# Kernel tuning notes

Measured on AMD Instinct MI355X. Metric: run time of the kernel, lower is better.

Reference implementation:

```python
import jax, jax.numpy as jnp
import numpy as np
import math

NUM_HEADS = 16
D_EMBED = 1024
D_HEAD = D_EMBED // NUM_HEADS


def setup_inputs() -> dict:
    key = jax.random.key(0)
    k1, k2, k3 = jax.random.split(key, 3)
    B, S = 4, 2048
    x = jax.random.normal(k1, (B, S, D_EMBED), dtype=jnp.float32)
    # Kaiming-ish init for the fused QKV and output projections
    scale_in = 1.0 / math.sqrt(D_EMBED)
    in_proj_weight = jax.random.normal(k2, (3 * D_EMBED, D_EMBED), dtype=jnp.float32) * scale_in
    out_proj_weight = jax.random.normal(k3, (D_EMBED, D_EMBED), dtype=jnp.float32) * scale_in
    return {
        "x": x,
        "in_proj_weight": in_proj_weight,
        "out_proj_weight": out_proj_weight,
        "causal_mask": 1,
    }


def reference(x, in_proj_weight, out_proj_weight, causal_mask):
    B, S, D = x.shape
    # fused QKV projection: x @ W_in^T -> [B, S, 3D], then split
    qkv = jnp.einsum("bsd,ed->bse", x, in_proj_weight)
    q, k, v = jnp.split(qkv, 3, axis=-1)
    # [B, S, H, dh] -> [B, H, S, dh]
    def to_heads(t):
        return t.reshape(B, S, NUM_HEADS, D_HEAD).transpose(0, 2, 1, 3)
    q, k, v = to_heads(q), to_heads(k), to_heads(v)
    # scores: [B, H, S, S]
    scores = jnp.einsum("bhqd,bhkd->bhqk", q, k) / math.sqrt(D_HEAD)
    if causal_mask:
        mask = jnp.triu(jnp.ones((S, S), dtype=bool), k=1)
        scores = jnp.where(mask, -jnp.inf, scores)
    attn = jax.nn.softmax(scores, axis=-1)
    out = jnp.einsum("bhqk,bhkd->bhqd", attn, v)
    out = out.transpose(0, 2, 1, 3).reshape(B, S, D)
    return jnp.einsum("bsd,ed->bse", out, out_proj_weight)
```

## Files before the change

kernel.cpp:

```cpp
#include <hip/hip_runtime.h>
#include <hip/hip_bf16.h>
#include <stdint.h>

typedef unsigned short u16;
typedef __attribute__((ext_vector_type(8))) short short8;
typedef __attribute__((ext_vector_type(4))) float floatx4;
typedef __attribute__((ext_vector_type(16))) float floatx16;
typedef __attribute__((ext_vector_type(4))) unsigned uint4v;
typedef __attribute__((ext_vector_type(2))) unsigned uint2v;

#define DEV static __device__ __forceinline__

DEV u16 f2bf(float f) {
  __hip_bfloat16 h = __float2bfloat16(f);
  return __builtin_bit_cast(u16, h);
}

DEV float fexp2(float x) {
  float r;
  asm("v_exp_f32 %0, %1" : "=v"(r) : "v"(x));
  return r;
}

DEV unsigned cvtpk(float lo, float hi) {
  unsigned r;
  asm("v_cvt_pk_bf16_f32 %0, %1, %2" : "=v"(r) : "v"(lo), "v"(hi));
  return r;
}

DEV void pswap(unsigned& a, unsigned& b) {
  uint2v r = __builtin_amdgcn_permlane32_swap(a, b, false, false);
  a = r[0];
  b = r[1];
}

DEV void cross32(float v, float& x, float& y) {
  unsigned a = __builtin_bit_cast(unsigned, v), b = a;
  pswap(a, b);
  x = __builtin_bit_cast(float, a);
  y = __builtin_bit_cast(float, b);
}

DEV floatx4 mfma16(short8 a, short8 b, floatx4 c) {
  return __builtin_amdgcn_mfma_f32_16x16x32_bf16(a, b, c, 0, 0, 0);
}
DEV floatx16 mfma32(short8 a, short8 b, floatx16 c) {
  return __builtin_amdgcn_mfma_f32_32x32x16_bf16(a, b, c, 0, 0, 0);
}

DEV void gload_lds16(const void* g, void* l) {
  __builtin_amdgcn_global_load_lds(
      (void __attribute__((address_space(1)))*)(g),
      (void __attribute__((address_space(3)))*)(l),
      16, 0, 0);
}

__global__ void cast3_kernel(const float* __restrict__ x, const float* __restrict__ win,
                             const float* __restrict__ wout,
                             u16* __restrict__ xb, u16* __restrict__ winb,
                             u16* __restrict__ woutb) {
  int i = blockIdx.x * 256 + threadIdx.x;
  const float* src;
  u16* dst;
  int off;
  if (i < 2097152) {
    src = x; dst = xb; off = i;
  } else if (i < 2883584) {
    src = win; dst = winb; off = i - 2097152;
  } else {
    src = wout; dst = woutb; off = i - 2883584;
  }
  float4 v = reinterpret_cast<const float4*>(src)[off];
  ushort4 o;
  o.x = f2bf(v.x); o.y = f2bf(v.y); o.z = f2bf(v.z); o.w = f2bf(v.w);
  reinterpret_cast<ushort4*>(dst)[off] = o;
}

template <int MODE>
__global__ __launch_bounds__(512, 2)
void gemm_bt(const u16* __restrict__ A, const u16* __restrict__ W,
             int M, int N, int K,
             u16* __restrict__ Qb, u16* __restrict__ Kb, u16* __restrict__ Vb,
             float* __restrict__ C) {
  __shared__ u16 As[3][128 * 64];
  __shared__ u16 Bs[3][256 * 64];
  const int tid = threadIdx.x;
  const int wave = tid >> 6, lane = tid & 63;
  const int lr = lane & 15, lg = lane >> 4;
  const int m0 = blockIdx.y * 128, n0 = blockIdx.x * 256;
  const int mq0 = (wave >> 2) * 64, nq0 = (wave & 3) * 64;

  floatx4 acc[4][4];
#pragma unroll
  for (int i = 0; i < 4; ++i)
#pragma unroll
    for (int j = 0; j < 4; ++j) acc[i][j] = (floatx4)0.f;

  const int NT = K >> 6;

  auto stage_a = [&](int t, int bi) {
#pragma unroll
    for (int i = 0; i < 2; ++i) {
      int s = i * 512 + tid;
      int row = s >> 3;
      int col = ((s & 7) ^ (row & 7)) * 8;
      gload_lds16(&A[(size_t)(m0 + row) * K + t * 64 + col], &As[bi][(size_t)s * 8]);
    }
  };
  auto stage_b = [&](int t, int bi, int i0, int i1) {
#pragma unroll 4
    for (int i = i0; i < i1; ++i) {
      int s = i * 512 + tid;
      int row = s >> 3;
      int col = ((s & 7) ^ (row & 7)) * 8;
      gload_lds16(&W[(size_t)(n0 + row) * K + t * 64 + col], &Bs[bi][(size_t)s * 8]);
    }
  };

  stage_a(0, 0);
  stage_b(0, 0, 0, 4);
  stage_a(1, 1);
  stage_b(1, 1, 0, 4);

  int bi = 0;
  for (int t = 0; t < NT; ++t) {
    if (t < NT - 1) {
      asm volatile("s_waitcnt vmcnt(6)" ::: "memory");
    } else {
      asm volatile("s_waitcnt vmcnt(0)" ::: "memory");
    }
    __builtin_amdgcn_sched_barrier(0);
    __builtin_amdgcn_s_barrier();
    __builtin_amdgcn_sched_barrier(0);

    int b2 = bi + 2; if (b2 >= 3) b2 -= 3;
    const bool do_st = (t + 2 < NT);

    short8 af[4][2], bf01[2][2];
#pragma unroll
    for (int i = 0; i < 4; ++i) {
      int row = mq0 + i * 16 + lr;
#pragma unroll
      for (int kh = 0; kh < 2; ++kh)
        af[i][kh] = *reinterpret_cast<const short8*>(
            &As[bi][row * 64 + (((kh * 4 + lg) ^ (row & 7)) * 8)]);
    }
#pragma unroll
    for (int j = 0; j < 2; ++j) {
      int row = nq0 + j * 16 + lr;
#pragma unroll
      for (int kh = 0; kh < 2; ++kh)
        bf01[j][kh] = *reinterpret_cast<const short8*>(
            &Bs[bi][row * 64 + (((kh * 4 + lg) ^ (row & 7)) * 8)]);
    }
    if (do_st) {
      stage_a(t + 2, b2);
      stage_b(t + 2, b2, 0, 1);
    }
    __builtin_amdgcn_sched_barrier(0);
    __builtin_amdgcn_s_setprio(1);
#pragma unroll
    for (int kh = 0; kh < 2; ++kh)
#pragma unroll
      for (int i = 0; i < 4; ++i)
#pragma unroll
        for (int j = 0; j < 2; ++j)
          acc[i][j] = mfma16(af[i][kh], bf01[j][kh], acc[i][j]);
    __builtin_amdgcn_s_setprio(0);
    __builtin_amdgcn_sched_barrier(0);
    __builtin_amdgcn_s_barrier();

    short8 bf23[2][2];
#pragma unroll
    for (int j = 0; j < 2; ++j) {
      int row = nq0 + (j + 2) * 16 + lr;
#pragma unroll
      for (int kh = 0; kh < 2; ++kh)
        bf23[j][kh] = *reinterpret_cast<const short8*>(
            &Bs[bi][row * 64 + (((kh * 4 + lg) ^ (row & 7)) * 8)]);
    }
    if (do_st) stage_b(t + 2, b2, 1, 4);
    __builtin_amdgcn_sched_barrier(0);
    __builtin_amdgcn_s_setprio(1);
#pragma unroll
    for (int kh = 0; kh < 2; ++kh)
#pragma unroll
      for (int i = 0; i < 4; ++i)
#pragma unroll
        for (int j = 0; j < 2; ++j)
          acc[i][j + 2] = mfma16(af[i][kh], bf23[j][kh], acc[i][j + 2]);
    __builtin_amdgcn_s_setprio(0);
    __builtin_amdgcn_sched_barrier(0);

    if (++bi == 3) bi = 0;
  }

  if (MODE == 0) {
#pragma unroll
    for (int j = 0; j < 4; ++j) {
      int n = n0 + nq0 + j * 16 + lr;
      int which = n >> 10;
      int d = n & 1023;
      int h = d >> 6, dh = d & 63;
      u16* dst = (which == 0) ? Qb : ((which == 1) ? Kb : Vb);
      float scale = (which == 0) ? 0.18033688f : 1.0f;
#pragma unroll
      for (int i = 0; i < 4; ++i) {
#pragma unroll
        for (int r = 0; r < 4; ++r) {
          int m = m0 + mq0 + i * 16 + lg * 4 + r;
          int b = m >> 11, s = m & 2047;
          dst[((size_t)(b * 16 + h) * 2048 + s) * 64 + dh] = f2bf(acc[i][j][r] * scale);
        }
      }
    }
  } else {
#pragma unroll
    for (int i = 0; i < 4; ++i)
#pragma unroll
      for (int j = 0; j < 4; ++j)
#pragma unroll
        for (int r = 0; r < 4; ++r) {
          int m = m0 + mq0 + i * 16 + lg * 4 + r;
          int n = n0 + nq0 + j * 16 + lr;
          C[(size_t)m * N + n] = acc[i][j][r];
        }
  }
}

__global__ __launch_bounds__(256, 2)
void attn_kernel(const u16* __restrict__ Qb, const u16* __restrict__ Kb,
                 const u16* __restrict__ Vb, u16* __restrict__ Ob) {
  const int lid = (int)blockIdx.x + 8 * (int)blockIdx.y;
  const int xcd = lid & 7;
  const int kk = lid >> 3;
  const int bh = xcd * 8 + (kk & 7);
  const int bx = kk >> 3;
  const u16* Qh = Qb + (size_t)bh * 2048 * 64;
  const u16* Kh = Kb + (size_t)bh * 2048 * 64;
  const u16* Vh = Vb + (size_t)bh * 2048 * 64;

  __shared__ u16 smem[3][8192];

  const int tid = threadIdx.x, wave = tid >> 6, lane = tid & 63;
  const int ln31 = lane & 31, hi = lane >> 5;
  const int swz = (lane & 7) * 8;
  const int b = bh >> 4, h = bh & 15;

  const int vp = tid & 31, vc8 = tid >> 5;

  auto stage_k = [&](int kvbase, u16* buf) {
#pragma unroll
    for (int i = 0; i < 2; ++i) {
      int s = i * 256 + tid;
      int row = s >> 3;
      int col = ((s & 7) ^ (row & 7)) * 8;
      gload_lds16(&Kh[(size_t)(kvbase + row) * 64 + col], &buf[(size_t)s * 8]);
    }
  };
  auto load_v = [&](int kvbase, short8& v0, short8& v1) {
    v0 = *reinterpret_cast<const short8*>(&Vh[(size_t)(kvbase + 2 * vp) * 64 + vc8 * 8]);
    v1 = *reinterpret_cast<const short8*>(&Vh[(size_t)(kvbase + 2 * vp + 1) * 64 + vc8 * 8]);
  };
  auto write_v = [&](u16* buf, short8 v0, short8 v1) {
#pragma unroll
    for (int j = 0; j < 8; ++j) {
      int d = vc8 * 8 + j;
      uint32_t pk = (uint32_t)(u16)v0[j] | ((uint32_t)(u16)v1[j] << 16);
      *reinterpret_cast<uint32_t*>(&buf[4096 + d * 64 + ((2 * vp) ^ ((d & 7) * 8))]) = pk;
    }
  };

  for (int ph = 0; ph < 2; ++ph) {
    const int tq = ph ? (15 - bx) : bx;
    const int q0w = tq * 128 + wave * 32;
    const int qrow = q0w + ln31;

    short8 qf[4];
#pragma unroll
    for (int c = 0; c < 4; ++c)
      qf[c] = *reinterpret_cast<const short8*>(
          &Qh[(size_t)qrow * 64 + c * 16 + hi * 8]);

    floatx16 accO0 = (floatx16)0.f, accO1 = (floatx16)0.f;
    float m_run = -1e30f, l_run = 0.f;

    auto do_qk = [&](int kvq, floatx16& SQ0, floatx16& SQ1, const u16* Ksq) {
      if (kvq > q0w + 31) return;
      SQ0 = (floatx16)0.f;
      SQ1 = (floatx16)0.f;
      __builtin_amdgcn_s_setprio(1);
#pragma unroll
      for (int c = 0; c < 4; ++c) {
        short8 kfA = *reinterpret_cast<const short8*>(
            &Ksq[ln31 * 64 + ((c * 16 + hi * 8) ^ swz)]);
        short8 kfB = *reinterpret_cast<const short8*>(
            &Ksq[(32 + ln31) * 64 + ((c * 16 + hi * 8) ^ swz)]);
        SQ0 = mfma32(kfA, qf[c], SQ0);
        SQ1 = mfma32(kfB, qf[c], SQ1);
      }
      __builtin_amdgcn_s_setprio(0);
    };

    auto do_smpv = [&](int kv0_, floatx16& SS0, floatx16& SS1, const u16* bufv) {
      if (kv0_ > q0w + 31) return;
      if (kv0_ + 63 > q0w) {
#pragma unroll
        for (int reg = 0; reg < 16; ++reg) {
          int kvA = kv0_ + (reg & 3) + 8 * (reg >> 2) + 4 * hi;
          if (kvA > qrow) SS0[reg] = -1e30f;
          if (kvA + 32 > qrow) SS1[reg] = -1e30f;
        }
      }
      float m8[8];
#pragma unroll
      for (int i = 0; i < 8; ++i)
        m8[i] = fmaxf(fmaxf(SS0[i], SS0[i + 8]), fmaxf(SS1[i], SS1[i + 8]));
      float mx = fmaxf(fmaxf(fmaxf(m8[0], m8[1]), fmaxf(m8[2], m8[3])),
                       fmaxf(fmaxf(m8[4], m8[5]), fmaxf(m8[6], m8[7])));
      {
        float xa, xb;
        cross32(mx, xa, xb);
        mx = fmaxf(xa, xb);
      }
      bool small_ = (mx <= m_run + 8.f);
      if (!__all(small_)) {
        float mn = fmaxf(m_run, mx);
        float fac = fexp2(m_run - mn);
        m_run = mn;
        l_run *= fac;
        accO0 *= fac;
        accO1 *= fac;
      }
#pragma unroll
      for (int i = 0; i < 16; ++i) SS0[i] = fexp2(SS0[i] - m_run);
#pragma unroll
      for (int i = 0; i < 16; ++i) SS1[i] = fexp2(SS1[i] - m_run);
      float a8[8];
#pragma unroll
      for (int i = 0; i < 8; ++i)
        a8[i] = (SS0[i] + SS0[i + 8]) + (SS1[i] + SS1[i + 8]);
      float rs = ((a8[0] + a8[1]) + (a8[2] + a8[3])) + ((a8[4] + a8[5]) + (a8[6] + a8[7]));
      {
        float xa, xb;
        cross32(rs, xa, xb);
        rs = xa + xb;
      }
      l_run += rs;
      short8 pf[4];
#define BUILD_PF(idx, S, base)                                        \
      {                                                               \
        unsigned u01 = cvtpk(S[base + 0], S[base + 1]);               \
        unsigned u23 = cvtpk(S[base + 2], S[base + 3]);               \
        unsigned u45 = cvtpk(S[base + 4], S[base + 5]);               \
        unsigned u67 = cvtpk(S[base + 6], S[base + 7]);               \
        pswap(u01, u45);                                              \
        pswap(u23, u67);                                              \
        uint4v w; w.x = u01; w.y = u23; w.z = u45; w.w = u67;         \
        pf[idx] = __builtin_bit_cast(short8, w);                      \
      }
      BUILD_PF(0, SS0, 0)
      BUILD_PF(1, SS0, 8)
      BUILD_PF(2, SS1, 0)
      BUILD_PF(3, SS1, 8)
#undef BUILD_PF
      const u16* Vt = bufv + 4096;
      __builtin_amdgcn_s_setprio(1);
#pragma unroll
      for (int c = 0; c < 4; ++c) {
        short8 vfA = *reinterpret_cast<const short8*>(
            &Vt[ln31 * 64 + ((c * 16 + hi * 8) ^ swz)]);
        short8 vfB = *reinterpret_cast<const short8*>(
            &Vt[(32 + ln31) * 64 + ((c * 16 + hi * 8) ^ swz)]);
        accO0 = mfma32(vfA, pf[c], accO0);
        accO1 = mfma32(vfB, pf[c], accO1);
      }
      __builtin_amdgcn_s_setprio(0);
    };

    const int nt = 2 * (tq + 1);

    __syncthreads();
    stage_k(0, smem[0]);
    {
      short8 v0, v1;
      load_v(0, v0, v1);
      write_v(smem[0], v0, v1);
    }
    stage_k(64, smem[1]);
    {
      short8 v0, v1;
      load_v(64, v0, v1);
      write_v(smem[1], v0, v1);
    }
    __syncthreads();

    floatx16 SA0, SA1, SB0, SB1;
    do_qk(0, SA0, SA1, smem[0]);

    for (int it = 0; it < nt; it += 2) {
      {
        const int kvc = it * 64;
        short8 nv0, nv1;
        const bool do_st = (it + 2) < nt;
        u16* sbuf = smem[(it + 2) % 3];
        if (do_st) {
          stage_k(kvc + 128, sbuf);
          load_v(kvc + 128, nv0, nv1);
        }
        do_qk(kvc + 64, SB0, SB1, smem[(it + 1) % 3]);
        do_smpv(kvc, SA0, SA1, smem[it % 3]);
        if (do_st) write_v(sbuf, nv0, nv1);
        __syncthreads();
      }
      {
        const int kvc = it * 64 + 64;
        short8 nv0, nv1;
        const bool do_st = (it + 3) < nt;
        u16* sbuf = smem[(it + 3) % 3];
        if (do_st) {
          stage_k(kvc + 128, sbuf);
          load_v(kvc + 128, nv0, nv1);
        }
        if (it + 2 < nt) do_qk(kvc + 64, SA0, SA1, smem[(it + 2) % 3]);
        do_smpv(kvc, SB0, SB1, smem[(it + 1) % 3]);
        if (do_st) write_v(sbuf, nv0, nv1);
        __syncthreads();
      }
    }

    u16* ep = &smem[0][0] + wave * 2048;
    float inv = 1.0f / l_run;
#define EPI_W(ACC, dh2)                                               \
    {                                                                 \
      _Pragma("unroll")                                               \
      for (int rp = 0; rp < 8; ++rp) {                                \
        int reg = rp * 2;                                             \
        unsigned pk = cvtpk(ACC[reg] * inv, ACC[reg + 1] * inv);      \
        int d = dh2 * 32 + (reg & 3) + 8 * (reg >> 2) + 4 * hi;       \
        *reinterpret_cast<uint32_t*>(                                 \
            &ep[ln31 * 64 + (d ^ ((ln31 & 7) * 8))]) = pk;            \
      }                                                               \
    }
    EPI_W(accO0, 0)
    EPI_W(accO1, 1)
#undef EPI_W
#pragma unroll
    for (int g = 0; g < 4; ++g) {
      int d0 = hi * 32 + g * 8;
      short8 o8 = *reinterpret_cast<const short8*>(
          &ep[ln31 * 64 + (d0 ^ ((ln31 & 7) * 8))]);
      *reinterpret_cast<short8*>(
          &Ob[(size_t)(b * 2048 + q0w + ln31) * 1024 + h * 64 + d0]) = o8;
    }
  }
}

extern "C" void kernel_launch(void* const* d_in, const int* in_sizes, int n_in,
                              void* d_out, int out_size, void* d_ws, size_t ws_size,
                              hipStream_t stream) {
  const float* x    = (const float*)d_in[0];
  const float* win  = (const float*)d_in[1];
  const float* wout = (const float*)d_in[2];
  float* out = (float*)d_out;

  char* ws = (char*)d_ws;
  u16* xb    = (u16*)(ws + 0);
  u16* winb  = (u16*)(ws + 16777216);
  u16* woutb = (u16*)(ws + 23068672);
  u16* Qb    = (u16*)(ws + 25165824);
  u16* Kb    = (u16*)(ws + 41943040);
  u16* Vb    = (u16*)(ws + 58720256);
  u16* Ob    = (u16*)(ws + 75497472);

  cast3_kernel<<<12288, 256, 0, stream>>>(x, win, wout, xb, winb, woutb);

  gemm_bt<0><<<dim3(12, 64), 512, 0, stream>>>(xb, winb, 8192, 3072, 1024,
                                               Qb, Kb, Vb, nullptr);
  attn_kernel<<<dim3(8, 64), 256, 0, stream>>>(Qb, Kb, Vb, Ob);
  gemm_bt<1><<<dim3(4, 64), 512, 0, stream>>>(Ob, woutb, 8192, 1024, 1024,
                                              nullptr, nullptr, nullptr, out);
}
```

Baseline: 163.6 us.

## Restructure attention KV loop to double-buffered 128-row tiles

Replaces the triple-buffered 64-row K/V pipeline, which software-pipelined QK of the next tile against softmax-PV of the current one, with a double-buffered scheme that stages 128 KV rows per iteration. Each iteration now runs QK and softmax-PV sequentially for two 64-row halves, with one barrier per 128 rows. This halves the number of barriers and raises LDS to 64KB per block, but loses the QK/softmax interleaving and holds more V registers in flight, which may hurt occupancy or latency hiding.

```diff
diff --git a/kernel.cpp b/kernel.cpp
--- a/kernel.cpp
+++ b/kernel.cpp
@@ -240,7 +240,7 @@
   const u16* Kh = Kb + (size_t)bh * 2048 * 64;
   const u16* Vh = Vb + (size_t)bh * 2048 * 64;
 
-  __shared__ u16 smem[3][8192];
+  __shared__ u16 smem[2][16384];
 
   const int tid = threadIdx.x, wave = tid >> 6, lane = tid & 63;
   const int ln31 = lane & 31, hi = lane >> 5;
@@ -251,7 +251,7 @@
 
   auto stage_k = [&](int kvbase, u16* buf) {
 #pragma unroll
-    for (int i = 0; i < 2; ++i) {
+    for (int i = 0; i < 4; ++i) {
       int s = i * 256 + tid;
       int row = s >> 3;
       int col = ((s & 7) ^ (row & 7)) * 8;
@@ -262,12 +262,12 @@
     v0 = *reinterpret_cast<const short8*>(&Vh[(size_t)(kvbase + 2 * vp) * 64 + vc8 * 8]);
     v1 = *reinterpret_cast<const short8*>(&Vh[(size_t)(kvbase + 2 * vp + 1) * 64 + vc8 * 8]);
   };
-  auto write_v = [&](u16* buf, short8 v0, short8 v1) {
+  auto write_v = [&](u16* vbuf, short8 v0, short8 v1) {
 #pragma unroll
     for (int j = 0; j < 8; ++j) {
       int d = vc8 * 8 + j;
       uint32_t pk = (uint32_t)(u16)v0[j] | ((uint32_t)(u16)v1[j] << 16);
-      *reinterpret_cast<uint32_t*>(&buf[4096 + d * 64 + ((2 * vp) ^ ((d & 7) * 8))]) = pk;
+      *reinterpret_cast<uint32_t*>(&vbuf[d * 64 + ((2 * vp) ^ ((d & 7) * 8))]) = pk;
     }
   };
 
@@ -302,7 +302,7 @@
       __builtin_amdgcn_s_setprio(0);
     };
 
-    auto do_smpv = [&](int kv0_, floatx16& SS0, floatx16& SS1, const u16* bufv) {
+    auto do_smpv = [&](int kv0_, floatx16& SS0, floatx16& SS1, const u16* Vt) {
       if (kv0_ > q0w + 31) return;
       if (kv0_ + 63 > q0w) {
 #pragma unroll
@@ -364,7 +364,6 @@
       BUILD_PF(2, SS1, 0)
       BUILD_PF(3, SS1, 8)
 #undef BUILD_PF
-      const u16* Vt = bufv + 4096;
       __builtin_amdgcn_s_setprio(1);
 #pragma unroll
       for (int c = 0; c < 4; ++c) {
@@ -378,55 +377,45 @@
       __builtin_amdgcn_s_setprio(0);
     };
 
-    const int nt = 2 * (tq + 1);
+    const int ntt = tq + 1;
 
     __syncthreads();
     stage_k(0, smem[0]);
     {
       short8 v0, v1;
       load_v(0, v0, v1);
-      write_v(smem[0], v0, v1);
-    }
-    stage_k(64, smem[1]);
-    {
-      short8 v0, v1;
+      write_v(smem[0] + 8192, v0, v1);
       load_v(64, v0, v1);
-      write_v(smem[1], v0, v1);
+      write_v(smem[0] + 12288, v0, v1);
     }
     __syncthreads();
 
-    floatx16 SA0, SA1, SB0, SB1;
-    do_qk(0, SA0, SA1, smem[0]);
-
-    for (int it = 0; it < nt; it += 2) {
+    for (int t = 0; t < ntt; ++t) {
+      const int kvb = t * 128;
+      short8 nva0, nva1, nvb0, nvb1;
+      const bool do_st = (t + 1) < ntt;
+      u16* sbuf = smem[(t + 1) & 1];
+      if (do_st) {
+        stage_k(kvb + 128, sbuf);
+        load_v(kvb + 128, nva0, nva1);
+        load_v(kvb + 192, nvb0, nvb1);
+      }
+      u16* cur = smem[t & 1];
       {
-        const int kvc = it * 64;
-        short8 nv0, nv1;
-        const bool do_st = (it + 2) < nt;
-        u16* sbuf = smem[(it + 2) % 3];
-        if (do_st) {
-          stage_k(kvc + 128, sbuf);
-          load_v(kvc + 128, nv0, nv1);
-        }
-        do_qk(kvc + 64, SB0, SB1, smem[(it + 1) % 3]);
-        do_smpv(kvc, SA0, SA1, smem[it % 3]);
-        if (do_st) write_v(sbuf, nv0, nv1);
-        __syncthreads();
+        floatx16 S0, S1;
+        do_qk(kvb, S0, S1, cur);
+        do_smpv(kvb, S0, S1, cur + 8192);
       }
       {
-        const int kvc = it * 64 + 64;
-        short8 nv0, nv1;
-        const bool do_st = (it + 3) < nt;
-        u16* sbuf = smem[(it + 3) % 3];
-        if (do_st) {
-          stage_k(kvc + 128, sbuf);
-          load_v(kvc + 128, nv0, nv1);
-        }
-        if (it + 2 < nt) do_qk(kvc + 64, SA0, SA1, smem[(it + 2) % 3]);
-        do_smpv(kvc, SB0, SB1, smem[(it + 1) % 3]);
-        if (do_st) write_v(sbuf, nv0, nv1);
-        __syncthreads();
-      }
+        floatx16 S0, S1;
+        do_qk(kvb + 64, S0, S1, cur + 4096);
+        do_smpv(kvb + 64, S0, S1, cur + 12288);
+      }
+      if (do_st) {
+        write_v(sbuf + 8192, nva0, nva1);
+        write_v(sbuf + 12288, nvb0, nvb1);
+      }
+      __syncthreads();
     }
 
     u16* ep = &smem[0][0] + wave * 2048;
```

New measurement: 164.1 us. About the same (+0.3%).
